# Optimization experiments

Measured on AMD Instinct MI355X. Metric: run time of the kernel, lower is better.

The kernel has to match this reference:

```python
import jax, jax.numpy as jnp
import numpy as np

B, NQ, NK, E, H, F, L = 8, 300, 4096, 256, 8, 2048, 6
D = E // H
SCALE = D ** -0.5


def _ln(x, g, b):
    m = x.mean(-1, keepdims=True)
    v = ((x - m) ** 2).mean(-1, keepdims=True)
    return (x - m) / jnp.sqrt(v + 1e-5) * g + b


def _split_heads(x):
    b, n, _ = x.shape
    return x.reshape(b, n, H, D).transpose(0, 2, 1, 3)  # (B,H,N,D)


def _merge_heads(x):
    b, h, n, d = x.shape
    return x.transpose(0, 2, 1, 3).reshape(b, n, h * d)


def setup_inputs() -> dict:
    key = jax.random.key(0)
    c = [0]
    def nk():
        c[0] += 1
        return jax.random.fold_in(key, c[0])
    def p(shape):
        return jax.random.normal(nk(), shape, jnp.float32) * 0.02
    return {
        "tgt": jax.random.normal(nk(), (B, NQ, E), jnp.float32),
        "memory": jax.random.normal(nk(), (B, NK, E), jnp.float32),
        "geometry_mask": jax.random.randint(nk(), (B, NQ, NK), 0, 2).astype(bool),
        "sa_wqkv": p((L, 3 * E, E)), "sa_bqkv": p((L, 3 * E)),
        "sa_wo": p((L, E, E)), "sa_bo": p((L, E)),
        "ca_wq": p((L, E, E)), "ca_bq": p((L, E)),
        "ca_wk": p((L, E, E)), "ca_bk": p((L, E)),
        "ca_wv": p((L, E, E)), "ca_bv": p((L, E)),
        "ca_wo": p((L, E, E)), "ca_bo": p((L, E)),
        "f_w1": p((L, F, E)), "f_b1": p((L, F)),
        "f_w2": p((L, E, F)), "f_b2": p((L, E)),
        "ln1g": jnp.ones((L, E)), "ln1b": jnp.zeros((L, E)),
        "ln2g": jnp.ones((L, E)), "ln2b": jnp.zeros((L, E)),
        "ln3g": jnp.ones((L, E)), "ln3b": jnp.zeros((L, E)),
        "lnfg": jnp.ones((E,)), "lnfb": jnp.zeros((E,)),
    }


def _forward(tgt, memory, geometry_mask, params):
    mask4 = geometry_mask[:, None, :, :]  # (B,1,NQ,NK), broadcast over heads

    def step(t, p):
        (wqkv, bqkv, wo, bo, wq, bq, wk, bk, wv, bv, wco, bco,
         w1, b1, w2, b2, g1, be1, g2, be2, g3, be3) = p
        # --- self-attention (torch nn.MultiheadAttention, eval mode) ---
        qkv = t @ wqkv.T + bqkv
        q, k, v = jnp.split(qkv, 3, axis=-1)
        q, k, v = _split_heads(q), _split_heads(k), _split_heads(v)
        a = jax.nn.softmax(jnp.einsum('bhqd,bhkd->bhqk', q, k) * SCALE, axis=-1)
        sa = _merge_heads(jnp.einsum('bhqk,bhkd->bhqd', a, v)) @ wo.T + bo
        t = _ln(t + sa, g1, be1)
        # --- geometry-constrained cross-attention ---
        q = _split_heads(t @ wq.T + bq)
        k = _split_heads(memory @ wk.T + bk)
        v = _split_heads(memory @ wv.T + bv)
        s = jnp.einsum('bhqd,bhkd->bhqk', q, k) * SCALE
        s = jnp.where(mask4, s, -jnp.inf)  # masked_fill(~mask, -inf)
        a = jax.nn.softmax(s, axis=-1)
        ca = _merge_heads(jnp.einsum('bhqk,bhkd->bhqd', a, v)) @ wco.T + bco
        t = _ln(t + ca, g2, be2)
        # --- FFN ---
        f = jax.nn.relu(t @ w1.T + b1) @ w2.T + b2
        t = _ln(t + f, g3, be3)
        return t, None

    out, _ = jax.lax.scan(step, tgt, params)
    return out


def reference(tgt, memory, geometry_mask, sa_wqkv, sa_bqkv, sa_wo, sa_bo,
              ca_wq, ca_bq, ca_wk, ca_bk, ca_wv, ca_bv, ca_wo, ca_bo,
              f_w1, f_b1, f_w2, f_b2, ln1g, ln1b, ln2g, ln2b, ln3g, ln3b,
              lnfg, lnfb):
    params = (sa_wqkv, sa_bqkv, sa_wo, sa_bo, ca_wq, ca_bq, ca_wk, ca_bk,
              ca_wv, ca_bv, ca_wo, ca_bo, f_w1, f_b1, f_w2, f_b2,
              ln1g, ln1b, ln2g, ln2b, ln3g, ln3b)
    out = _forward(tgt, memory, geometry_mask, params)
    return _ln(out, lnfg, lnfb)
```

## Files before the change

kernel.cpp:

```cpp
#include <hip/hip_runtime.h>
#include <hip/hip_bf16.h>

constexpr int cB = 8, cNQ = 300, cNK = 4096, cE = 256, cH = 8, cD = 32, cF = 2048, cL = 6;
constexpr int MT = cB * cNQ;
constexpr int MM = cB * cNK;
constexpr int cQT = 10;
constexpr int cKS = 4;
constexpr float kScale = 0.17677669529663687f;
constexpr float kC2 = 0.25506601f;

typedef __attribute__((ext_vector_type(8))) short short8_t;
typedef __attribute__((ext_vector_type(4))) short short4_t;
typedef __attribute__((ext_vector_type(4))) float float4_t;

__device__ inline short f2bf(float x) {
  __hip_bfloat16 h = __float2bfloat16(x);
  return __builtin_bit_cast(short, h);
}

__global__ void init_t(const float* __restrict__ in, float* __restrict__ t,
                       __hip_bfloat16* __restrict__ tb, int n) {
  int i = blockIdx.x * 256 + threadIdx.x;
  if (i < n) { float v = in[i]; t[i] = v; tb[i] = __float2bfloat16(v); }
}
__global__ void cast_f32_bf16(const float* __restrict__ in, __hip_bfloat16* __restrict__ out, int n) {
  int i = blockIdx.x * 256 + threadIdx.x;
  if (i < n) out[i] = __float2bfloat16(in[i]);
}

__global__ void pack_mask_T(const int* __restrict__ m, unsigned* __restrict__ mT) {
  int key = blockIdx.x * 256 + threadIdx.x;
  int qt = blockIdx.y, b = blockIdx.z;
  unsigned w = 0;
  for (int j = 0; j < 32; ++j) {
    int q = qt * 32 + j;
    unsigned bit = (q < cNQ) ? (unsigned)(m[((size_t)b * cNQ + q) * cNK + key] != 0) : 0u;
    w |= bit << j;
  }
  mT[((size_t)b * cQT + qt) * cNK + key] = w;
}

template<typename TA, typename TW, int EPI, int OMODE, typename TOUT>
__global__ __launch_bounds__(256) void gemm_mfma(const TA* __restrict__ A,
                                                 const TW* __restrict__ W,
                                                 const float* __restrict__ bias,
                                                 TOUT* __restrict__ C,
                                                 int M, int N, int K) {
  constexpr int LDSS = 72;
  __shared__ short As[64][LDSS];
  __shared__ short Ws[64][LDSS];
  int tid = threadIdx.x;
  int bm = blockIdx.x * 64, bn = blockIdx.y * 64;
  int lane = tid & 63, wave = tid >> 6;
  int m16 = lane & 15, quad = lane >> 4;
  int wm = (wave >> 1) * 32, wn = (wave & 1) * 32;

  int srow = tid >> 2;
  int kc = (tid & 3) * 16;
  bool aok = (bm + srow) < M;

  float4_t acc[2][2];
#pragma unroll
  for (int i = 0; i < 2; ++i)
#pragma unroll
    for (int j = 0; j < 2; ++j) acc[i][j] = (float4_t){0.f, 0.f, 0.f, 0.f};

  for (int k0 = 0; k0 < K; k0 += 64) {
    if constexpr (__hip_internal::is_same<TA, float>::value) {
      const float* src = A + (size_t)(bm + srow) * K + k0 + kc;
      short8_t p0, p1;
#pragma unroll
      for (int u = 0; u < 8; ++u) p0[u] = aok ? f2bf(src[u]) : (short)0;
#pragma unroll
      for (int u = 0; u < 8; ++u) p1[u] = aok ? f2bf(src[8 + u]) : (short)0;
      *(short8_t*)&As[srow][kc] = p0;
      *(short8_t*)&As[srow][kc + 8] = p1;
    } else {
      const TA* src = A + (size_t)(bm + srow) * K + k0 + kc;
      short8_t z = 0;
      *(short8_t*)&As[srow][kc] = aok ? *(const short8_t*)src : z;
      *(short8_t*)&As[srow][kc + 8] = aok ? *(const short8_t*)(src + 8) : z;
    }
    if constexpr (__hip_internal::is_same<TW, float>::value) {
      const float* src = W + (size_t)(bn + srow) * K + k0 + kc;
      short8_t p0, p1;
#pragma unroll
      for (int u = 0; u < 8; ++u) p0[u] = f2bf(src[u]);
#pragma unroll
      for (int u = 0; u < 8; ++u) p1[u] = f2bf(src[8 + u]);
      *(short8_t*)&Ws[srow][kc] = p0;
      *(short8_t*)&Ws[srow][kc + 8] = p1;
    } else {
      const TW* src = W + (size_t)(bn + srow) * K + k0 + kc;
      *(short8_t*)&Ws[srow][kc] = *(const short8_t*)src;
      *(short8_t*)&Ws[srow][kc + 8] = *(const short8_t*)(src + 8);
    }
    __syncthreads();
#pragma unroll
    for (int kk = 0; kk < 2; ++kk) {
      short8_t aF[2], bF[2];
#pragma unroll
      for (int i = 0; i < 2; ++i)
        aF[i] = *(const short8_t*)&As[wm + i * 16 + m16][kk * 32 + quad * 8];
#pragma unroll
      for (int j = 0; j < 2; ++j)
        bF[j] = *(const short8_t*)&Ws[wn + j * 16 + m16][kk * 32 + quad * 8];
#pragma unroll
      for (int i = 0; i < 2; ++i)
#pragma unroll
        for (int j = 0; j < 2; ++j)
          acc[i][j] = __builtin_amdgcn_mfma_f32_16x16x32_bf16(aF[i], bF[j], acc[i][j], 0, 0, 0);
    }
    __syncthreads();
  }

  if constexpr (OMODE == 2) {
#pragma unroll
    for (int i = 0; i < 2; ++i)
#pragma unroll
      for (int r = 0; r < 4; ++r) {
        int ml = wm + i * 16 + quad * 4 + r;
#pragma unroll
        for (int j = 0; j < 2; ++j) {
          int nl = wn + j * 16 + m16;
          Ws[nl][ml] = f2bf(acc[i][j][r] + bias[bn + nl]);
        }
      }
    __syncthreads();
    int nl = tid >> 2, mc = (tid & 3) * 16;
    if (bm + mc < M) {
      int n = bn + nl;
      __hip_bfloat16* dst = (__hip_bfloat16*)C +
          ((size_t)(n >> 5) * 32 + (n & 31)) * (size_t)M + bm + mc;
      *(short8_t*)dst = *(const short8_t*)&Ws[nl][mc];
      *(short8_t*)(dst + 8) = *(const short8_t*)&Ws[nl][mc + 8];
    }
  } else {
#pragma unroll
    for (int i = 0; i < 2; ++i) {
#pragma unroll
      for (int r = 0; r < 4; ++r) {
        int m = bm + wm + i * 16 + quad * 4 + r;
        if (m >= M) continue;
#pragma unroll
        for (int j = 0; j < 2; ++j) {
          int n = bn + wn + j * 16 + m16;
          float v = acc[i][j][r] + bias[n];
          if (EPI == 1) v = fmaxf(v, 0.f);
          if (EPI == 2 && n < 256) v *= kC2;
          if (EPI == 3) v *= kC2;
          if constexpr (OMODE == 1) {
            ((__hip_bfloat16*)C)[((size_t)(n >> 5) * M + m) * 32 + (n & 31)] = __float2bfloat16(v);
          } else if constexpr (__hip_internal::is_same<TOUT, float>::value) {
            C[(size_t)m * N + n] = v;
          } else {
            C[(size_t)m * N + n] = __float2bfloat16(v);
          }
        }
      }
    }
  }
}

template<typename TW, int EPI, typename TOUT>
__global__ __launch_bounds__(256) void gemm32(const __hip_bfloat16* __restrict__ A,
                                              const TW* __restrict__ W,
                                              const float* __restrict__ bias,
                                              TOUT* __restrict__ C,
                                              int M, int N, int K) {
  __shared__ short As[32][72];
  __shared__ short Ws[64][72];
  int tid = threadIdx.x;
  int bm = blockIdx.x * 32, bn = blockIdx.y * 64;
  int lane = tid & 63, wave = tid >> 6;
  int m16 = lane & 15, quad = lane >> 4;
  int wn = wave * 16;

  int sa_row = tid >> 3, sa_c = (tid & 7) * 8;
  int sw_row = tid >> 2, sw_c = (tid & 3) * 16;
  bool aok = (bm + sa_row) < M;

  float4_t acc[2];
  acc[0] = (float4_t){0.f, 0.f, 0.f, 0.f};
  acc[1] = (float4_t){0.f, 0.f, 0.f, 0.f};

  for (int k0 = 0; k0 < K; k0 += 64) {
    {
      const __hip_bfloat16* src = A + (size_t)(bm + sa_row) * K + k0 + sa_c;
      short8_t z = 0;
      *(short8_t*)&As[sa_row][sa_c] = aok ? *(const short8_t*)src : z;
    }
    if constexpr (__hip_internal::is_same<TW, float>::value) {
      const float* src = W + (size_t)(bn + sw_row) * K + k0 + sw_c;
      short8_t p0, p1;
#pragma unroll
      for (int u = 0; u < 8; ++u) p0[u] = f2bf(src[u]);
#pragma unroll
      for (int u = 0; u < 8; ++u) p1[u] = f2bf(src[8 + u]);
      *(short8_t*)&Ws[sw_row][sw_c] = p0;
      *(short8_t*)&Ws[sw_row][sw_c + 8] = p1;
    } else {
      const TW* src = W + (size_t)(bn + sw_row) * K + k0 + sw_c;
      *(short8_t*)&Ws[sw_row][sw_c] = *(const short8_t*)src;
      *(short8_t*)&Ws[sw_row][sw_c + 8] = *(const short8_t*)(src + 8);
    }
    __syncthreads();
#pragma unroll
    for (int kk = 0; kk < 2; ++kk) {
      short8_t aF[2], bF;
#pragma unroll
      for (int i = 0; i < 2; ++i)
        aF[i] = *(const short8_t*)&As[i * 16 + m16][kk * 32 + quad * 8];
      bF = *(const short8_t*)&Ws[wn + m16][kk * 32 + quad * 8];
#pragma unroll
      for (int i = 0; i < 2; ++i)
        acc[i] = __builtin_amdgcn_mfma_f32_16x16x32_bf16(aF[i], bF, acc[i], 0, 0, 0);
    }
    __syncthreads();
  }

#pragma unroll
  for (int i = 0; i < 2; ++i) {
#pragma unroll
    for (int r = 0; r < 4; ++r) {
      int m = bm + i * 16 + quad * 4 + r;
      if (m >= M) continue;
      int n = bn + wn + m16;
      float v = acc[i][r] + bias[n];
      if (EPI == 1) v = fmaxf(v, 0.f);
      if (EPI == 3) v *= kC2;
      if constexpr (__hip_internal::is_same<TOUT, float>::value) {
        C[(size_t)m * N + n] = v;
      } else {
        C[(size_t)m * N + n] = __float2bfloat16(v);
      }
    }
  }
}

template<typename TW, int EPI, int OMODE, typename TOUT>
__global__ __launch_bounds__(256) void gemm128(const __hip_bfloat16* __restrict__ A,
                                               const TW* __restrict__ W,
                                               const float* __restrict__ bias,
                                               TOUT* __restrict__ C,
                                               int M, int N, int K) {
  __shared__ short lds[2 * 128 * 72];
  auto As = (short(*)[72])lds;
  auto Ws = (short(*)[72])(lds + 128 * 72);
  int tid = threadIdx.x;
  int bm = blockIdx.x * 128, bn = blockIdx.y * 128;
  int lane = tid & 63, wave = tid >> 6;
  int n16 = lane & 15, quad = lane >> 4;
  int wm = (wave >> 1) * 64, wn = (wave & 1) * 64;
  int srow = tid >> 1, kc = (tid & 1) * 32;
  bool aok = (bm + srow) < M;

  float4_t acc[4][4];
#pragma unroll
  for (int i = 0; i < 4; ++i)
#pragma unroll
    for (int j = 0; j < 4; ++j) acc[i][j] = (float4_t){0.f, 0.f, 0.f, 0.f};

  for (int k0 = 0; k0 < K; k0 += 64) {
    {
      const __hip_bfloat16* src = A + (size_t)(bm + srow) * K + k0 + kc;
      short8_t z = 0;
#pragma unroll
      for (int u = 0; u < 4; ++u)
        *(short8_t*)&As[srow][kc + u * 8] = aok ? *(const short8_t*)(src + u * 8) : z;
    }
    if constexpr (__hip_internal::is_same<TW, float>::value) {
      const float* src = W + (size_t)(bn + srow) * K + k0 + kc;
#pragma unroll
      for (int u = 0; u < 4; ++u) {
        short8_t p;
#pragma unroll
        for (int v = 0; v < 8; ++v) p[v] = f2bf(src[u * 8 + v]);
        *(short8_t*)&Ws[srow][kc + u * 8] = p;
      }
    } else {
      const TW* src = W + (size_t)(bn + srow) * K + k0 + kc;
#pragma unroll
      for (int u = 0; u < 4; ++u)
        *(short8_t*)&Ws[srow][kc + u * 8] = *(const short8_t*)(src + u * 8);
    }
    __syncthreads();
#pragma unroll
    for (int kk = 0; kk < 2; ++kk) {
      short8_t aF[4], bF[4];
#pragma unroll
      for (int i = 0; i < 4; ++i)
        aF[i] = *(const short8_t*)&As[wm + i * 16 + n16][kk * 32 + quad * 8];
#pragma unroll
      for (int j = 0; j < 4; ++j)
        bF[j] = *(const short8_t*)&Ws[wn + j * 16 + n16][kk * 32 + quad * 8];
#pragma unroll
      for (int i = 0; i < 4; ++i)
#pragma unroll
        for (int j = 0; j < 4; ++j)
          acc[i][j] = __builtin_amdgcn_mfma_f32_16x16x32_bf16(aF[i], bF[j], acc[i][j], 0, 0, 0);
    }
    __syncthreads();
  }

  if constexpr (OMODE == 2) {
    auto TT = (short(*)[128])lds;
#pragma unroll
    for (int i = 0; i < 4; ++i)
#pragma unroll
      for (int r = 0; r < 4; ++r) {
        int ml = wm + i * 16 + quad * 4 + r;
#pragma unroll
        for (int j = 0; j < 4; ++j) {
          int nl = wn + j * 16 + n16;
          TT[nl][ml] = f2bf(acc[i][j][r] + bias[bn + nl]);
        }
      }
    __syncthreads();
    int nl = tid >> 1, mh = (tid & 1) * 64;
    int n = bn + nl;
    __hip_bfloat16* dst = (__hip_bfloat16*)C +
        ((size_t)(n >> 5) * 32 + (n & 31)) * (size_t)M + bm + mh;
#pragma unroll
    for (int ch = 0; ch < 8; ++ch) {
      if (bm + mh + ch * 8 < M)
        *(short8_t*)(dst + ch * 8) = *(const short8_t*)&TT[nl][mh + ch * 8];
    }
  } else {
#pragma unroll
    for (int i = 0; i < 4; ++i) {
#pragma unroll
      for (int r = 0; r < 4; ++r) {
        int m = bm + wm + i * 16 + quad * 4 + r;
        if (m >= M) continue;
#pragma unroll
        for (int j = 0; j < 4; ++j) {
          int n = bn + wn + j * 16 + n16;
          float v = acc[i][j][r] + bias[n];
          if (EPI == 1) v = fmaxf(v, 0.f);
          if constexpr (OMODE == 1) {
            ((__hip_bfloat16*)C)[((size_t)(n >> 5) * M + m) * 32 + (n & 31)] = __float2bfloat16(v);
          } else if constexpr (__hip_internal::is_same<TOUT, float>::value) {
            C[(size_t)m * N + n] = v;
          } else {
            C[(size_t)m * N + n] = __float2bfloat16(v);
          }
        }
      }
    }
  }
}

template<typename TQ, bool MASKED, bool SPLIT>
__global__ __launch_bounds__(256) void attn_flash(
    const TQ* __restrict__ qb, size_t strQb, size_t strQh, int qRowStr,
    const __hip_bfloat16* __restrict__ kb, size_t strKb, size_t strKh, int kRowStr,
    const __hip_bfloat16* __restrict__ vt, size_t strVb, size_t strVh, size_t strVd,
    const unsigned* __restrict__ mT, size_t strMb,
    float* __restrict__ pO, size_t pStrO,
    float* __restrict__ pL, size_t pStrL,
    __hip_bfloat16* __restrict__ outF,
    int nq, int nk, int kChunk) {
  int hb = blockIdx.x;
  int h = hb & 7, bz = hb >> 3;
  int qt = blockIdx.y, ks = blockIdx.z;
  int qbase = qt * 32;

  const TQ* q = qb + (size_t)bz * strQb + (size_t)h * strQh;
  const __hip_bfloat16* K = kb + (size_t)bz * strKb + (size_t)h * strKh;
  const __hip_bfloat16* V = vt + (size_t)bz * strVb + (size_t)h * strVh;
  const unsigned* mrow = MASKED ? (mT + (size_t)bz * strMb + (size_t)qt * cNK) : nullptr;

  int tid = threadIdx.x;
  int lane = tid & 63, wave = tid >> 6;
  int n16 = lane & 15, quad = lane >> 4;

  __shared__ float redO[4][32][33];
  __shared__ float redL[4][32];
  short* sPw = (short*)&redO[0][0][0] + wave * (32 * 40);

  short8_t qf[2];
#pragma unroll
  for (int qi = 0; qi < 2; ++qi) {
    qf[qi] = 0;
    int qr = qbase + qi * 16 + n16;
    if (qr < nq) {
      const TQ* qp = q + (size_t)qr * qRowStr + quad * 8;
      if constexpr (__hip_internal::is_same<TQ, float>::value) {
#pragma unroll
        for (int j = 0; j < 8; ++j) qf[qi][j] = f2bf(qp[j]);
      } else {
        qf[qi] = *(const short8_t*)qp;
      }
    }
  }
  short8_t ones;
#pragma unroll
  for (int j = 0; j < 8; ++j) ones[j] = f2bf(1.0f);

  float4_t accO[2][2], accL[2];
#pragma unroll
  for (int qi = 0; qi < 2; ++qi) {
    accL[qi] = (float4_t){0.f, 0.f, 0.f, 0.f};
#pragma unroll
    for (int di = 0; di < 2; ++di) accO[qi][di] = (float4_t){0.f, 0.f, 0.f, 0.f};
  }
  float4_t zero4 = {0.f, 0.f, 0.f, 0.f};

  int kpad = (nk + 31) & ~31;
  int kbeg = ks * kChunk + wave * 32;
  int kend = ks * kChunk + kChunk;
  if (kend > kpad) kend = kpad;

  short8_t ka0, ka1, va0, va1, kb0, kb1, vb0, vb1;
  unsigned wa0 = 0, wa1 = 0, wb0 = 0, wb1 = 0;
  float oa0 = 1.f, oa1 = 1.f, ob0 = 1.f, ob1 = 1.f;

#define ATTN_LOAD(KF0, KF1, VF0, VF1, W0, W1, O0, O1, KO)                          \
  {                                                                                \
    int k0_ = (KO) + 2 * n16;                                                      \
    if (MASKED) {                                                                  \
      uint2 mw_ = *(const uint2*)(mrow + k0_);                                     \
      W0 = mw_.x; W1 = mw_.y;                                                      \
    } else {                                                                       \
      O0 = (k0_ < nk) ? 1.f : 0.f;                                                 \
      O1 = (k0_ + 1 < nk) ? 1.f : 0.f;                                             \
    }                                                                              \
    KF0 = *(const short8_t*)(K + (size_t)k0_ * kRowStr + quad * 8);                \
    KF1 = *(const short8_t*)(K + (size_t)(k0_ + 1) * kRowStr + quad * 8);          \
    VF0 = *(const short8_t*)(V + (size_t)n16 * strVd + (KO) + quad * 8);           \
    VF1 = *(const short8_t*)(V + (size_t)(16 + n16) * strVd + (KO) + quad * 8);    \
  }

#define ATTN_COMPUTE(CK0, CK1, CV0, CV1, CW0, CW1, CO0, CO1)                       \
  {                                                                                \
    float4_t s00 = __builtin_amdgcn_mfma_f32_16x16x32_bf16(qf[0], CK0, zero4, 0, 0, 0); \
    float4_t s01 = __builtin_amdgcn_mfma_f32_16x16x32_bf16(qf[0], CK1, zero4, 0, 0, 0); \
    float4_t s10 = __builtin_amdgcn_mfma_f32_16x16x32_bf16(qf[1], CK0, zero4, 0, 0, 0); \
    float4_t s11 = __builtin_amdgcn_mfma_f32_16x16x32_bf16(qf[1], CK1, zero4, 0, 0, 0); \
    _Pragma("unroll")                                                              \
    for (int qi = 0; qi < 2; ++qi) {                                               \
      const float4_t& sa = qi ? s10 : s00;                                         \
      const float4_t& sb = qi ? s11 : s01;                                         \
      _Pragma("unroll")                                                            \
      for (int r = 0; r < 4; ++r) {                                                \
        int row_ = qi * 16 + quad * 4 + r;                                         \
        float e0_, e1_;                                                            \
        asm("v_exp_f32 %0, %1" : "=v"(e0_) : "v"(sa[r]));                          \
        asm("v_exp_f32 %0, %1" : "=v"(e1_) : "v"(sb[r]));                          \
        float m0_, m1_;                                                            \
        if (MASKED) {                                                              \
          m0_ = (float)((CW0 >> row_) & 1u);                                       \
          m1_ = (float)((CW1 >> row_) & 1u);                                       \
        } else {                                                                   \
          m0_ = CO0; m1_ = CO1;                                                    \
        }                                                                          \
        e0_ *= m0_; e1_ *= m1_;                                                    \
        unsigned pw_;                                                              \
        asm("v_cvt_pk_bf16_f32 %0, %1, %2" : "=v"(pw_) : "v"(e0_), "v"(e1_));      \
        *(unsigned*)&sPw[row_ * 40 + 2 * n16] = pw_;                               \
      }                                                                            \
    }                                                                              \
    _Pragma("unroll")                                                              \
    for (int qi = 0; qi < 2; ++qi) {                                               \
      short8_t pf = *(const short8_t*)&sPw[(qi * 16 + n16) * 40 + quad * 8];       \
      accO[qi][0] = __builtin_amdgcn_mfma_f32_16x16x32_bf16(pf, CV0, accO[qi][0], 0, 0, 0); \
      accO[qi][1] = __builtin_amdgcn_mfma_f32_16x16x32_bf16(pf, CV1, accO[qi][1], 0, 0, 0); \
      accL[qi]    = __builtin_amdgcn_mfma_f32_16x16x32_bf16(pf, ones, accL[qi], 0, 0, 0);   \
    }                                                                              \
  }

  int ko = kbeg;
  if (ko < kend) {
    ATTN_LOAD(ka0, ka1, va0, va1, wa0, wa1, oa0, oa1, ko);
    while (true) {
      int nx = ko + 128;
      if (nx < kend) ATTN_LOAD(kb0, kb1, vb0, vb1, wb0, wb1, ob0, ob1, nx);
      ATTN_COMPUTE(ka0, ka1, va0, va1, wa0, wa1, oa0, oa1);
      ko = nx;
      if (ko >= kend) break;
      nx = ko + 128;
      if (nx < kend) ATTN_LOAD(ka0, ka1, va0, va1, wa0, wa1, oa0, oa1, nx);
      ATTN_COMPUTE(kb0, kb1, vb0, vb1, wb0, wb1, ob0, ob1);
      ko = nx;
      if (ko >= kend) break;
    }
  }
#undef ATTN_LOAD
#undef ATTN_COMPUTE

  __syncthreads();
#pragma unroll
  for (int qi = 0; qi < 2; ++qi) {
#pragma unroll
    for (int r = 0; r < 4; ++r) {
      int row = qi * 16 + quad * 4 + r;
#pragma unroll
      for (int di = 0; di < 2; ++di)
        redO[wave][row][di * 16 + n16] = accO[qi][di][r];
      if (n16 == 0) redL[wave][row] = accL[qi][r];
    }
  }
  __syncthreads();

  int row = tid >> 3, c0 = (tid & 7) * 4;
  if constexpr (SPLIT) {
    size_t oBase = (size_t)ks * pStrO + (size_t)(bz * cNQ) * 256 + h * 32;
    if (qbase + row < nq) {
      float4_t o;
#pragma unroll
      for (int u = 0; u < 4; ++u)
        o[u] = redO[0][row][c0 + u] + redO[1][row][c0 + u] +
               redO[2][row][c0 + u] + redO[3][row][c0 + u];
      *(float4_t*)&pO[oBase + (size_t)(qbase + row) * 256 + c0] = o;
    }
    if (tid < 32 && qbase + tid < nq) {
      float l = redL[0][tid] + redL[1][tid] + redL[2][tid] + redL[3][tid];
      pL[(size_t)ks * pStrL + (size_t)hb * 320 + qbase + tid] = l;
    }
  } else {
    if (qbase + row < nq) {
      float l = redL[0][row] + redL[1][row] + redL[2][row] + redL[3][row];
      float inv = 1.f / l;
      float o[4];
#pragma unroll
      for (int u = 0; u < 4; ++u)
        o[u] = (redO[0][row][c0 + u] + redO[1][row][c0 + u] +
                redO[2][row][c0 + u] + redO[3][row][c0 + u]) * inv;
      short4_t res = {f2bf(o[0]), f2bf(o[1]), f2bf(o[2]), f2bf(o[3])};
      *(short4_t*)&outF[(size_t)(bz * cNQ + qbase + row) * 256 + h * 32 + c0] = res;
    }
  }
}

__global__ __launch_bounds__(64) void attn_merge(const float* __restrict__ pO,
                                                 const float* __restrict__ pL,
                                                 __hip_bfloat16* __restrict__ out) {
  int row = blockIdx.x;
  int lane = threadIdx.x;
  int c0 = lane * 4;
  int bz = row / cNQ, qq = row - bz * cNQ;
  int h = c0 >> 5;
  float l = 0.f;
#pragma unroll
  for (int ks = 0; ks < cKS; ++ks)
    l += pL[(size_t)ks * (64 * 320) + (size_t)(bz * 8 + h) * 320 + qq];
  float inv = 1.f / l;
  float o[4] = {0.f, 0.f, 0.f, 0.f};
#pragma unroll
  for (int ks = 0; ks < cKS; ++ks) {
    const float4_t v = *(const float4_t*)&pO[(size_t)ks * (MT * 256) + (size_t)row * 256 + c0];
#pragma unroll
    for (int u = 0; u < 4; ++u) o[u] += v[u];
  }
  short4_t res = {f2bf(o[0] * inv), f2bf(o[1] * inv), f2bf(o[2] * inv), f2bf(o[3] * inv)};
  *(short4_t*)&out[(size_t)row * 256 + c0] = res;
}

__global__ __launch_bounds__(64) void add_ln_k(float* __restrict__ t,
                                               __hip_bfloat16* __restrict__ tb,
                                               const float* __restrict__ delta,
                                               const float* __restrict__ g,
                                               const float* __restrict__ bb) {
  int r = blockIdx.x, lane = threadIdx.x;
  size_t base = (size_t)r * cE + lane * 4;
  float x[4];
  float s = 0.f;
#pragma unroll
  for (int i = 0; i < 4; ++i) { x[i] = t[base + i] + delta[base + i]; s += x[i]; }
  for (int off = 32; off; off >>= 1) s += __shfl_xor(s, off);
  float mean = s * (1.f / cE);
  float v = 0.f;
#pragma unroll
  for (int i = 0; i < 4; ++i) { float dd = x[i] - mean; v += dd * dd; }
  for (int off = 32; off; off >>= 1) v += __shfl_xor(v, off);
  float rstd = rsqrtf(v * (1.f / cE) + 1e-5f);
  float y[4];
#pragma unroll
  for (int i = 0; i < 4; ++i) {
    y[i] = (x[i] - mean) * rstd * g[lane * 4 + i] + bb[lane * 4 + i];
    t[base + i] = y[i];
  }
  short4_t pb = {f2bf(y[0]), f2bf(y[1]), f2bf(y[2]), f2bf(y[3])};
  *(short4_t*)&tb[base] = pb;
}

__global__ __launch_bounds__(64) void final_ln_k(const float* __restrict__ t,
                                                 const float* __restrict__ g,
                                                 const float* __restrict__ bb,
                                                 float* __restrict__ out) {
  int r = blockIdx.x, lane = threadIdx.x;
  size_t base = (size_t)r * cE + lane * 4;
  float x[4];
  float s = 0.f;
#pragma unroll
  for (int i = 0; i < 4; ++i) { x[i] = t[base + i]; s += x[i]; }
  for (int off = 32; off; off >>= 1) s += __shfl_xor(s, off);
  float mean = s * (1.f / cE);
  float v = 0.f;
#pragma unroll
  for (int i = 0; i < 4; ++i) { float dd = x[i] - mean; v += dd * dd; }
  for (int off = 32; off; off >>= 1) v += __shfl_xor(v, off);
  float rstd = rsqrtf(v * (1.f / cE) + 1e-5f);
#pragma unroll
  for (int i = 0; i < 4; ++i)
    out[base + i] = (x[i] - mean) * rstd * g[lane * 4 + i] + bb[lane * 4 + i];
}

struct Bufs {
  float *t, *s1, *s2, *pO, *pL;
  __hip_bfloat16 *tb, *big2, *vtq, *saOut, *s2b, *qbf, *ffnh, *kbuf, *vtb, *membf;
  unsigned* mTr;
  const float* memory;
  bool fullKV, precast;
};

template<typename TW>
static void run_layers(const TW* const* wt, const float* const* bs,
                       const float* ln1g, const float* ln1b,
                       const float* ln2g, const float* ln2b,
                       const float* ln3g, const float* ln3b,
                       Bufs B, hipStream_t stream) {
  const size_t pStrO = (size_t)MT * 256, pStrL = 64 * 320;
  for (int l = 0; l < cL; ++l) {
    const TW* wqkv = wt[0] + (size_t)l * 3 * cE * cE;  const float* bqkv = bs[0] + (size_t)l * 3 * cE;
    const TW* wo   = wt[1] + (size_t)l * cE * cE;      const float* bo   = bs[1] + (size_t)l * cE;
    const TW* wq   = wt[2] + (size_t)l * cE * cE;      const float* bq   = bs[2] + (size_t)l * cE;
    const TW* wk   = wt[3] + (size_t)l * cE * cE;      const float* bk   = bs[3] + (size_t)l * cE;
    const TW* wv   = wt[4] + (size_t)l * cE * cE;      const float* bv   = bs[4] + (size_t)l * cE;
    const TW* wco  = wt[5] + (size_t)l * cE * cE;      const float* bco  = bs[5] + (size_t)l * cE;
    const TW* w1   = wt[6] + (size_t)l * cF * cE;      const float* b1   = bs[6] + (size_t)l * cF;
    const TW* w2   = wt[7] + (size_t)l * cE * cF;      const float* b2   = bs[7] + (size_t)l * cE;

    gemm_mfma<__hip_bfloat16, TW, 2, 0, __hip_bfloat16><<<dim3(38, 8), 256, 0, stream>>>(
        B.tb, wqkv, bqkv, B.big2, MT, 512, cE);
    gemm_mfma<__hip_bfloat16, TW, 0, 2, __hip_bfloat16><<<dim3(38, 4), 256, 0, stream>>>(
        B.tb, wqkv + (size_t)512 * cE, bqkv + 512, B.vtq, MT, cE, cE);
    attn_flash<__hip_bfloat16, false, false><<<dim3(64, cQT, 1), 256, 0, stream>>>(
        B.big2, (size_t)cNQ * 512, 32, 512,
        B.big2 + 256, (size_t)cNQ * 512, 32, 512,
        B.vtq, 300, (size_t)cD * MT, MT,
        nullptr, 0,
        B.pO, pStrO, B.pL, pStrL, B.saOut, cNQ, cNQ, 320);
    gemm32<TW, 0, float><<<dim3(75, 4), 256, 0, stream>>>(
        B.saOut, wo, bo, B.s2, MT, cE, cE);
    add_ln_k<<<MT, 64, 0, stream>>>(B.t, B.tb, B.s2, ln1g + (size_t)l * cE, ln1b + (size_t)l * cE);
    gemm32<TW, 3, __hip_bfloat16><<<dim3(75, 4), 256, 0, stream>>>(
        B.tb, wq, bq, B.qbf, MT, cE, cE);
    if (B.fullKV && B.precast) {
      gemm128<TW, 0, 1, __hip_bfloat16><<<dim3(256, 2), 256, 0, stream>>>(
          B.membf, wk, bk, B.kbuf, MM, cE, cE);
      gemm128<TW, 0, 2, __hip_bfloat16><<<dim3(256, 2), 256, 0, stream>>>(
          B.membf, wv, bv, B.vtb, MM, cE, cE);
      attn_flash<__hip_bfloat16, true, true><<<dim3(64, cQT, cKS), 256, 0, stream>>>(
          B.qbf, (size_t)cNQ * cE, 32, cE,
          B.kbuf, (size_t)cNK * cD, (size_t)MM * cD, cD,
          B.vtb, (size_t)cNK, (size_t)cD * MM, MM,
          B.mTr, (size_t)cQT * cNK,
          B.pO, pStrO, B.pL, pStrL, nullptr, cNQ, cNK, 1024);
      attn_merge<<<MT, 64, 0, stream>>>(B.pO, B.pL, B.s2b);
    } else {
      for (int b = 0; b < cB; ++b) {
        const float* memb = B.memory + (size_t)b * cNK * cE;
        gemm_mfma<float, TW, 0, 1, __hip_bfloat16><<<dim3(64, 4), 256, 0, stream>>>(
            memb, wk, bk, B.kbuf, cNK, cE, cE);
        gemm_mfma<float, TW, 0, 2, __hip_bfloat16><<<dim3(64, 4), 256, 0, stream>>>(
            memb, wv, bv, B.vtb, cNK, cE, cE);
        attn_flash<__hip_bfloat16, true, true><<<dim3(8, cQT, cKS), 256, 0, stream>>>(
            B.qbf + (size_t)b * cNQ * cE, 0, 32, cE,
            B.kbuf, 0, (size_t)cNK * cD, cD,
            B.vtb, 0, (size_t)cD * cNK, cNK,
            B.mTr + (size_t)b * cQT * cNK, 0,
            B.pO + (size_t)b * cNQ * 256, pStrO, B.pL + (size_t)b * 8 * 320, pStrL,
            nullptr, cNQ, cNK, 1024);
      }
      attn_merge<<<MT, 64, 0, stream>>>(B.pO, B.pL, B.s2b);
    }
    gemm32<TW, 0, float><<<dim3(75, 4), 256, 0, stream>>>(
        B.s2b, wco, bco, B.s1, MT, cE, cE);
    add_ln_k<<<MT, 64, 0, stream>>>(B.t, B.tb, B.s1, ln2g + (size_t)l * cE, ln2b + (size_t)l * cE);
    gemm128<TW, 1, 0, __hip_bfloat16><<<dim3(19, 16), 256, 0, stream>>>(
        B.tb, w1, b1, B.ffnh, MT, cF, cE);
    gemm32<TW, 0, float><<<dim3(75, 4), 256, 0, stream>>>(
        B.ffnh, w2, b2, B.s1, MT, cE, cF);
    add_ln_k<<<MT, 64, 0, stream>>>(B.t, B.tb, B.s1, ln3g + (size_t)l * cE, ln3b + (size_t)l * cE);
  }
}

extern "C" void kernel_launch(void* const* d_in, const int* in_sizes, int n_in,
                              void* d_out, int out_size, void* d_ws, size_t ws_size,
                              hipStream_t stream) {
  (void)in_sizes; (void)n_in; (void)out_size;
  const float* tgt    = (const float*)d_in[0];
  const float* memory = (const float*)d_in[1];
  const int*   gmask  = (const int*)d_in[2];
  const float* w_in[8]  = {(const float*)d_in[3], (const float*)d_in[5], (const float*)d_in[7],
                           (const float*)d_in[9], (const float*)d_in[11], (const float*)d_in[13],
                           (const float*)d_in[15], (const float*)d_in[17]};
  const float* b_in[8]  = {(const float*)d_in[4], (const float*)d_in[6], (const float*)d_in[8],
                           (const float*)d_in[10], (const float*)d_in[12], (const float*)d_in[14],
                           (const float*)d_in[16], (const float*)d_in[18]};
  const size_t w_sz[8]  = {(size_t)cL*3*cE*cE, (size_t)cL*cE*cE, (size_t)cL*cE*cE,
                           (size_t)cL*cE*cE, (size_t)cL*cE*cE, (size_t)cL*cE*cE,
                           (size_t)cL*cF*cE, (size_t)cL*cE*cF};
  const float* ln1g = (const float*)d_in[19], *ln1b = (const float*)d_in[20];
  const float* ln2g = (const float*)d_in[21], *ln2b = (const float*)d_in[22];
  const float* ln3g = (const float*)d_in[23], *ln3b = (const float*)d_in[24];
  const float* lnfg = (const float*)d_in[25], *lnfb = (const float*)d_in[26];

  char* wp = (char*)d_ws;
  auto alloc = [&](size_t bytes) { void* p = wp; wp += (bytes + 255) & ~(size_t)255; return p; };

  Bufs B;
  B.memory = memory;
  B.t  = (float*)alloc((size_t)MT * cE * 4);
  B.s1 = (float*)alloc((size_t)MT * cE * 4);
  B.s2 = (float*)alloc((size_t)MT * cE * 4);
  B.tb = (__hip_bfloat16*)alloc((size_t)MT * cE * 2);
  B.big2 = (__hip_bfloat16*)alloc((size_t)MT * 512 * 2);
  B.vtq  = (__hip_bfloat16*)alloc((size_t)cH * cD * MT * 2);
  B.mTr = (unsigned*)alloc((size_t)cB * cQT * cNK * 4);
  B.pO = (float*)alloc((size_t)cKS * MT * 256 * 4);
  B.pL = (float*)alloc((size_t)cKS * 64 * 320 * 4);
  B.saOut = (__hip_bfloat16*)B.pO;
  B.s2b = B.big2 + (size_t)MT * 256;
  B.qbf = (__hip_bfloat16*)B.s1;
  B.ffnh = (__hip_bfloat16*)B.pO;

  size_t kvFull = (size_t)cH * MM * cD * 2;
  size_t used = (size_t)(wp - (char*)d_ws);
  B.fullKV = ws_size >= used + 2 * kvFull;
  if (B.fullKV) {
    B.kbuf = (__hip_bfloat16*)alloc(kvFull);
    B.vtb  = (__hip_bfloat16*)alloc(kvFull);
  } else {
    B.kbuf = (__hip_bfloat16*)alloc((size_t)cH * cNK * cD * 2);
    B.vtb  = (__hip_bfloat16*)alloc((size_t)cH * cNK * cD * 2);
  }
  size_t memBytes = (size_t)MM * cE * 2;
  used = (size_t)(wp - (char*)d_ws);
  B.precast = B.fullKV && (ws_size >= used + memBytes);
  B.membf = B.precast ? (__hip_bfloat16*)alloc(memBytes) : nullptr;

  size_t wbfTotal = 0;
  for (int i = 0; i < 8; ++i) wbfTotal += ((w_sz[i] * 2 + 255) & ~(size_t)255);
  used = (size_t)(wp - (char*)d_ws);
  bool wPre = ws_size >= used + wbfTotal;
  __hip_bfloat16* wbf[8] = {};
  if (wPre)
    for (int i = 0; i < 8; ++i) wbf[i] = (__hip_bfloat16*)alloc(w_sz[i] * 2);

  init_t<<<(MT * cE + 255) / 256, 256, 0, stream>>>(tgt, B.t, B.tb, MT * cE);
  pack_mask_T<<<dim3(cNK / 256, cQT, cB), 256, 0, stream>>>(gmask, B.mTr);
  if (B.precast)
    cast_f32_bf16<<<(MM * cE + 255) / 256, 256, 0, stream>>>(memory, B.membf, MM * cE);
  if (wPre)
    for (int i = 0; i < 8; ++i)
      cast_f32_bf16<<<(int)((w_sz[i] + 255) / 256), 256, 0, stream>>>(w_in[i], wbf[i], (int)w_sz[i]);

  if (wPre) {
    const __hip_bfloat16* wt[8];
    for (int i = 0; i < 8; ++i) wt[i] = wbf[i];
    run_layers<__hip_bfloat16>(wt, b_in, ln1g, ln1b, ln2g, ln2b, ln3g, ln3b, B, stream);
  } else {
    run_layers<float>(w_in, b_in, ln1g, ln1b, ln2g, ln2b, ln3g, ln3b, B, stream);
  }

  final_ln_k<<<MT, 64, 0, stream>>>(B.t, lnfg, lnfb, (float*)d_out);
}
```

Measured before the change: 1.210 ms.

## Add dedicated cross-attention kernel processing all query tiles per block to reuse K/V

Replaces the generic flash-attention launch for masked cross-attention with a specialized kernel where each block owns one (batch, head, key-split) and loops over all 10 query tiles across its 4 waves. K and V tiles are loaded once into double-buffered shared memory and reused for every query tile, instead of being re-streamed per query tile. It uses a fixed-exponent softmax (no running max) with the row sum computed by an MFMA against a ones vector. The grid shrinks from 64x10x4 to 64x1x4 blocks, which reduces parallelism and leaves waves with unbalanced work (3 vs 2 tiles).

```diff
diff --git a/kernel.cpp b/kernel.cpp
--- a/kernel.cpp
+++ b/kernel.cpp
@@ -345,6 +345,154 @@
           } else {
             C[(size_t)m * N + n] = __float2bfloat16(v);
           }
+        }
+      }
+    }
+  }
+}
+
+__global__ __launch_bounds__(256) void attn_cross(
+    const __hip_bfloat16* __restrict__ qb,
+    const __hip_bfloat16* __restrict__ kb,
+    const __hip_bfloat16* __restrict__ vt,
+    const unsigned* __restrict__ mT,
+    float* __restrict__ pO,
+    float* __restrict__ pL) {
+  int hb = blockIdx.x, ks = blockIdx.z;
+  int h = hb & 7, bz = hb >> 3;
+  const __hip_bfloat16* Q = qb + (size_t)(bz * cNQ) * cE + h * cD;
+  const __hip_bfloat16* K = kb + ((size_t)h * MM + (size_t)bz * cNK) * cD;
+  const __hip_bfloat16* V = vt + (size_t)h * cD * MM + (size_t)bz * cNK;
+  const unsigned* mb = mT + (size_t)bz * (cQT * cNK);
+
+  int tid = threadIdx.x;
+  int lane = tid & 63, wave = tid >> 6;
+  int n16 = lane & 15, quad = lane >> 4;
+
+  __shared__ short Ks[2][64][40];
+  __shared__ short Vs[2][32][72];
+  __shared__ short sPa[4][32][40];
+  short* sPw = &sPa[wave][0][0];
+
+  int nt = (wave < 2) ? 3 : 2;
+
+  short8_t qf[3][2];
+#pragma unroll
+  for (int t = 0; t < 3; ++t) {
+    int qtt = wave + t * 4;
+#pragma unroll
+    for (int qi = 0; qi < 2; ++qi) {
+      qf[t][qi] = 0;
+      int qr = qtt * 32 + qi * 16 + n16;
+      if (t < nt && qr < cNQ)
+        qf[t][qi] = *(const short8_t*)(Q + (size_t)qr * cE + quad * 8);
+    }
+  }
+  short8_t ones;
+#pragma unroll
+  for (int j = 0; j < 8; ++j) ones[j] = f2bf(1.0f);
+
+  float4_t accO[3][2][2];
+  float4_t accL[3][2];
+#pragma unroll
+  for (int t = 0; t < 3; ++t)
+#pragma unroll
+    for (int qi = 0; qi < 2; ++qi) {
+      accL[t][qi] = (float4_t){0.f, 0.f, 0.f, 0.f};
+#pragma unroll
+      for (int di = 0; di < 2; ++di) accO[t][qi][di] = (float4_t){0.f, 0.f, 0.f, 0.f};
+    }
+  float4_t zero4 = {0.f, 0.f, 0.f, 0.f};
+
+  constexpr int CHUNK = cNK / cKS;
+  constexpr int NW = CHUNK / 64;
+  int kbeg = ks * CHUNK;
+
+  int krow = tid >> 2, kcol = (tid & 3) * 8;
+  int vrow = tid >> 3, vcol = (tid & 7) * 8;
+  short8_t kreg, vreg;
+
+#define CX_LDG(KO)                                                            \
+  {                                                                           \
+    kreg = *(const short8_t*)(K + (size_t)((KO) + krow) * cD + kcol);         \
+    vreg = *(const short8_t*)(V + (size_t)vrow * MM + (KO) + vcol);           \
+  }
+#define CX_STO(BUF)                                                           \
+  {                                                                           \
+    *(short8_t*)&Ks[BUF][krow][kcol] = kreg;                                  \
+    *(short8_t*)&Vs[BUF][vrow][vcol] = vreg;                                  \
+  }
+
+  CX_LDG(kbeg);
+  CX_STO(0);
+  __syncthreads();
+
+  for (int w = 0; w < NW; ++w) {
+    int cur = w & 1;
+    if (w + 1 < NW) CX_LDG(kbeg + (w + 1) * 64);
+#pragma unroll
+    for (int s = 0; s < 2; ++s) {
+      short8_t kf0 = *(const short8_t*)&Ks[cur][s * 32 + 2 * n16][quad * 8];
+      short8_t kf1 = *(const short8_t*)&Ks[cur][s * 32 + 2 * n16 + 1][quad * 8];
+      short8_t vf0 = *(const short8_t*)&Vs[cur][n16][s * 32 + quad * 8];
+      short8_t vf1 = *(const short8_t*)&Vs[cur][16 + n16][s * 32 + quad * 8];
+      int kabs = kbeg + w * 64 + s * 32 + 2 * n16;
+#pragma unroll
+      for (int t = 0; t < 3; ++t) {
+        if (t >= nt) continue;
+        int qtt = wave + t * 4;
+        uint2 mw = *(const uint2*)(mb + (size_t)qtt * cNK + kabs);
+        float4_t s00 = __builtin_amdgcn_mfma_f32_16x16x32_bf16(qf[t][0], kf0, zero4, 0, 0, 0);
+        float4_t s01 = __builtin_amdgcn_mfma_f32_16x16x32_bf16(qf[t][0], kf1, zero4, 0, 0, 0);
+        float4_t s10 = __builtin_amdgcn_mfma_f32_16x16x32_bf16(qf[t][1], kf0, zero4, 0, 0, 0);
+        float4_t s11 = __builtin_amdgcn_mfma_f32_16x16x32_bf16(qf[t][1], kf1, zero4, 0, 0, 0);
+#pragma unroll
+        for (int qi = 0; qi < 2; ++qi) {
+          const float4_t& sa = qi ? s10 : s00;
+          const float4_t& sb = qi ? s11 : s01;
+#pragma unroll
+          for (int r = 0; r < 4; ++r) {
+            int row = qi * 16 + quad * 4 + r;
+            float e0, e1;
+            asm("v_exp_f32 %0, %1" : "=v"(e0) : "v"(sa[r]));
+            asm("v_exp_f32 %0, %1" : "=v"(e1) : "v"(sb[r]));
+            e0 *= (float)((mw.x >> row) & 1u);
+            e1 *= (float)((mw.y >> row) & 1u);
+            unsigned pw;
+            asm("v_cvt_pk_bf16_f32 %0, %1, %2" : "=v"(pw) : "v"(e0), "v"(e1));
+            *(unsigned*)&sPw[row * 40 + 2 * n16] = pw;
+          }
+        }
+#pragma unroll
+        for (int qi = 0; qi < 2; ++qi) {
+          short8_t pf = *(const short8_t*)&sPw[(qi * 16 + n16) * 40 + quad * 8];
+          accO[t][qi][0] = __builtin_amdgcn_mfma_f32_16x16x32_bf16(pf, vf0, accO[t][qi][0], 0, 0, 0);
+          accO[t][qi][1] = __builtin_amdgcn_mfma_f32_16x16x32_bf16(pf, vf1, accO[t][qi][1], 0, 0, 0);
+          accL[t][qi]    = __builtin_amdgcn_mfma_f32_16x16x32_bf16(pf, ones, accL[t][qi], 0, 0, 0);
+        }
+      }
+    }
+    if (w + 1 < NW) CX_STO((w + 1) & 1);
+    __syncthreads();
+  }
+#undef CX_LDG
+#undef CX_STO
+
+  size_t oBase = (size_t)ks * ((size_t)MT * 256) + (size_t)(bz * cNQ) * 256 + h * 32;
+#pragma unroll
+  for (int t = 0; t < 3; ++t) {
+    if (t >= nt) continue;
+    int qtt = wave + t * 4;
+#pragma unroll
+    for (int qi = 0; qi < 2; ++qi) {
+#pragma unroll
+      for (int r = 0; r < 4; ++r) {
+        int row = qtt * 32 + qi * 16 + quad * 4 + r;
+        if (row < cNQ) {
+          pO[oBase + (size_t)row * 256 + n16]      = accO[t][qi][0][r];
+          pO[oBase + (size_t)row * 256 + 16 + n16] = accO[t][qi][1][r];
+          if (n16 == 0)
+            pL[(size_t)ks * (64 * 320) + (size_t)hb * 320 + row] = accL[t][qi][r];
         }
       }
     }
@@ -652,12 +800,8 @@
           B.membf, wk, bk, B.kbuf, MM, cE, cE);
       gemm128<TW, 0, 2, __hip_bfloat16><<<dim3(256, 2), 256, 0, stream>>>(
           B.membf, wv, bv, B.vtb, MM, cE, cE);
-      attn_flash<__hip_bfloat16, true, true><<<dim3(64, cQT, cKS), 256, 0, stream>>>(
-          B.qbf, (size_t)cNQ * cE, 32, cE,
-          B.kbuf, (size_t)cNK * cD, (size_t)MM * cD, cD,
-          B.vtb, (size_t)cNK, (size_t)cD * MM, MM,
-          B.mTr, (size_t)cQT * cNK,
-          B.pO, pStrO, B.pL, pStrL, nullptr, cNQ, cNK, 1024);
+      attn_cross<<<dim3(64, 1, cKS), 256, 0, stream>>>(
+          B.qbf, B.kbuf, B.vtb, B.mTr, B.pO, B.pL);
       attn_merge<<<MT, 64, 0, stream>>>(B.pO, B.pL, B.s2b);
     } else {
       for (int b = 0; b < cB; ++b) {
```

Result: slower. 1.285 ms (+6.2%).
